# Kernel tuning notes

Measured on AMD Instinct MI355X. Metric: run time of the kernel, lower is better.

The kernel has to match this reference:

```python
import jax, jax.numpy as jnp
import numpy as np


def _layernorm(x, g, b):
    # keras LayerNormalization default epsilon = 1e-3
    m = jnp.mean(x, axis=-1, keepdims=True)
    v = jnp.var(x, axis=-1, keepdims=True)
    return (x - m) * jax.lax.rsqrt(v + 1e-3) * g + b


def _gat(x, mask, W, a_src, a_dst, b):
    # PyG-style GATConv with concat heads, expressed densely over the
    # thresholded adjacency mask (edges where adj > 0.5; mask[i, j] = edge j->i).
    # x: [B, N, Din], W: [Din, H, C], mask: [N, N] bool
    h = jnp.einsum('bnd,dhc->bnhc', x, W)                 # [B,N,H,C]
    s_src = jnp.einsum('bnhc,hc->bhn', h, a_src)          # [B,H,N]
    s_dst = jnp.einsum('bnhc,hc->bhn', h, a_dst)          # [B,H,N]
    e = jax.nn.leaky_relu(s_dst[:, :, :, None] + s_src[:, :, None, :], 0.2)  # [B,H,i,j]
    e = jnp.where(mask[None, None], e, jnp.float32(-1e9))
    alpha = jax.nn.softmax(e, axis=-1)                    # softmax over neighbors j
    out = jnp.einsum('bhij,bjhc->bihc', alpha, h)         # aggregate messages
    B, N, H, C = out.shape
    return out.reshape(B, N, H * C) + b


def setup_inputs() -> dict:
    key = jax.random.key(0)
    ks = jax.random.split(key, 20)
    B, T, N, F = 4, 24, 500, 3
    HID, OUT, HEADS = 8, 16, 4      # SpatialProcessor(num_nodes, 3, 8, 16)
    D, AH, KD, FF = 16, 2, 8, 32    # EfficientTransformer(16, heads=2, ff_dim=32)
    n = lambda k, shape, sc=0.3: jax.random.normal(k, shape, dtype=jnp.float32) * sc
    z = lambda shape: jnp.zeros(shape, jnp.float32)
    return {
        'x': jax.random.normal(ks[0], (B, T, N, F), dtype=jnp.float32),
        'embedding': jax.random.normal(ks[1], (N, HID), dtype=jnp.float32),
        'proj_w': n(ks[2], (F, HID)), 'proj_b': z((HID,)),
        'g1_w': n(ks[3], (HID, HEADS, HID // HEADS)),
        'g1_as': n(ks[4], (HEADS, HID // HEADS)),
        'g1_ad': n(ks[5], (HEADS, HID // HEADS)),
        'g1_b': z((HID,)),
        'g2_w': n(ks[6], (HID, HEADS, OUT // HEADS)),
        'g2_as': n(ks[7], (HEADS, OUT // HEADS)),
        'g2_ad': n(ks[8], (HEADS, OUT // HEADS)),
        'g2_b': z((OUT,)),
        'wq': n(ks[9], (D, AH, KD)), 'bq': z((AH, KD)),
        'wk': n(ks[10], (D, AH, KD)), 'bk': z((AH, KD)),
        'wv': n(ks[11], (D, AH, KD)), 'bv': z((AH, KD)),
        'wo': n(ks[12], (AH, KD, D)), 'bo': z((D,)),
        'ln1_g': jnp.ones((D,), jnp.float32), 'ln1_b': z((D,)),
        'ln2_g': jnp.ones((D,), jnp.float32), 'ln2_b': z((D,)),
        'f_w1': n(ks[13], (D, FF)), 'f_b1': z((FF,)),
        'f_w2': n(ks[14], (FF, D)), 'f_b2': z((D,)),
        'r_w1': n(ks[15], (D, D)), 'r_b1': z((D,)),
        'r_w2': n(ks[16], (D, 1)), 'r_b2': z((1,)),
    }


def reference(x, embedding, proj_w, proj_b, g1_w, g1_as, g1_ad, g1_b,
              g2_w, g2_as, g2_ad, g2_b, wq, bq, wk, bk, wv, bv, wo, bo,
              ln1_g, ln1_b, ln2_g, ln2_b, f_w1, f_b1, f_w2, f_b2,
              r_w1, r_b1, r_w2, r_b2):
    B, T, N, F = x.shape
    # AdaptiveAdjacency: cosine similarity of learned node embeddings,
    # identical across batch; edges extracted where adj > 0.5 (diag is 1 -> self loops)
    ne = embedding * jax.lax.rsqrt(jnp.sum(embedding * embedding, -1, keepdims=True))
    adj = ne @ ne.T
    mask = adj > 0.5                                   # [N, N] bool
    # SpatialProcessor over B*T independent graphs
    h = x.reshape(B * T, N, F) @ proj_w + proj_b        # Dense proj -> [BT, N, 8]
    h = jax.nn.gelu(_gat(h, mask, g1_w, g1_as, g1_ad, g1_b), approximate=False)
    h = _gat(h, mask, g2_w, g2_as, g2_ad, g2_b)         # [BT, N, 16]
    D = h.shape[-1]
    # Faithful to original: raw tf.reshape [B,T,N,16] -> [B*N, T, 16] (no transpose)
    t = h.reshape(B * N, T, D)
    # keras MultiHeadAttention(heads=2, key_dim=8), 1 transformer layer
    q = jnp.einsum('bse,ehd->bshd', t, wq) + bq
    k = jnp.einsum('bse,ehd->bshd', t, wk) + bk
    v = jnp.einsum('bse,ehd->bshd', t, wv) + bv
    scale = jnp.sqrt(jnp.asarray(q.shape[-1], jnp.float32))
    att = jax.nn.softmax(jnp.einsum('bshd,bthd->bhst', q, k) / scale, axis=-1)
    o = jnp.einsum('bhst,bthd->bshd', att, v)
    o = jnp.einsum('bshd,hde->bse', o, wo) + bo
    t = _layernorm(t + o, ln1_g, ln1_b)
    ffn = jax.nn.gelu(t @ f_w1 + f_b1, approximate=False) @ f_w2 + f_b2
    t = _layernorm(t + ffn, ln2_g, ln2_b)
    pooled = t.reshape(B, N, T, D).mean(axis=2)
    r = jax.nn.gelu(pooled @ r_w1 + r_b1, approximate=False) @ r_w2 + r_b2
    return r[..., 0]
```

## Files before the change

### kernel.cpp

```cpp
#include <hip/hip_runtime.h>
#include <math.h>
#include <type_traits>

#define DEV __device__ __forceinline__

DEV float gelu_exact(float x) {
    return 0.5f * x * (1.0f + erff(x * 0.70710678118654752f));
}

__global__ __launch_bounds__(512)
void mask_kernel(const float* __restrict__ emb,
                 unsigned short* __restrict__ nbr,
                 int* __restrict__ deg) {
    const int i = blockIdx.x;
    const int j = threadIdx.x;
    float ei[8], ej[8];
    float si = 0.f, sj = 0.f;
#pragma unroll
    for (int e = 0; e < 8; ++e) { ei[e] = emb[i * 8 + e]; si += ei[e] * ei[e]; }
    const int jj = (j < 500) ? j : 0;
#pragma unroll
    for (int e = 0; e < 8; ++e) { ej[e] = emb[jj * 8 + e]; sj += ej[e] * ej[e]; }
    const float ri = 1.0f / sqrtf(si);
    const float rj = 1.0f / sqrtf(sj);
    float dot = 0.f;
#pragma unroll
    for (int e = 0; e < 8; ++e) dot += (ei[e] * ri) * (ej[e] * rj);
    const bool pred = (j < 500) && (dot > 0.5f);
    const unsigned long long m = __ballot(pred);

    __shared__ unsigned wcnt[8];
    const int wave = j >> 6, lane = j & 63;
    if (lane == 0) wcnt[wave] = (unsigned)__popcll(m);
    __syncthreads();
    unsigned off = 0;
    for (int w = 0; w < wave; ++w) off += wcnt[w];
    if (pred) {
        const unsigned pos = off + (unsigned)__popcll(m & ((1ull << lane) - 1ull));
        if (pos < 128) nbr[i * 128 + pos] = (unsigned short)j;
    }
    if (j == 0) {
        unsigned t = 0;
        for (int w = 0; w < 8; ++w) t += wcnt[w];
        deg[i] = (int)(t > 128u ? 128u : t);
    }
}

template <int C, int OUTS, bool PROJ, bool GELU_OUT>
__global__ __launch_bounds__(512)
void gat_kernel(const float* __restrict__ in,
                const float* __restrict__ pw,
                const float* __restrict__ pb,
                const float* __restrict__ W,
                const float* __restrict__ asrc,
                const float* __restrict__ adst,
                const float* __restrict__ bias,
                const unsigned short* __restrict__ nbr,
                const int* __restrict__ deg,
                float* __restrict__ out) {
    using Vec = std::conditional_t<C == 2, float2, float4>;
    constexpr int HSTR = (C == 2) ? 10 : 20;
    const int b = blockIdx.x >> 3;
    const int slice = blockIdx.x & 7;
    const int tid = threadIdx.x;
    __shared__ float h1[500 * HSTR];
    __shared__ float ssrc[4 * 516];

    if (tid < 500) {
        float xv[8];
        if constexpr (PROJ) {
            const float* xr = in + ((size_t)b * 500 + tid) * 3;
            const float x0 = xr[0], x1 = xr[1], x2 = xr[2];
#pragma unroll
            for (int e = 0; e < 8; ++e)
                xv[e] = x0 * pw[e] + x1 * pw[8 + e] + x2 * pw[16 + e] + pb[e];
        } else {
            const float4* xr = (const float4*)(in + ((size_t)b * 500 + tid) * 8);
            const float4 v0 = xr[0], v1 = xr[1];
            xv[0] = v0.x; xv[1] = v0.y; xv[2] = v0.z; xv[3] = v0.w;
            xv[4] = v1.x; xv[5] = v1.y; xv[6] = v1.z; xv[7] = v1.w;
        }
#pragma unroll
        for (int h = 0; h < 4; ++h) {
            float acc[C];
#pragma unroll
            for (int c = 0; c < C; ++c) acc[c] = 0.f;
#pragma unroll
            for (int e = 0; e < 8; ++e) {
                const float xe = xv[e];
#pragma unroll
                for (int c = 0; c < C; ++c) acc[c] += xe * W[(e * 4 + h) * C + c];
            }
            float ss = 0.f;
            Vec hv;
#pragma unroll
            for (int c = 0; c < C; ++c) ss += acc[c] * asrc[h * C + c];
            if constexpr (C == 2) { hv.x = acc[0]; hv.y = acc[1]; }
            else { hv.x = acc[0]; hv.y = acc[1]; hv.z = acc[2]; hv.w = acc[3]; }
            *(Vec*)&h1[tid * HSTR + h * C] = hv;
            ssrc[h * 516 + tid] = ss;
        }
    }
    __syncthreads();

    const int pairId = tid >> 1;
    const int half = tid & 1;
    const int h = pairId & 3;
    const int local = pairId >> 2;
    const int i = slice * 63 + local;
    const bool valid = (local < 63) && (i < 500);
    float num[C];
#pragma unroll
    for (int c = 0; c < C; ++c) num[c] = 0.f;
    float den = 0.f;
    if (valid) {
        float dd = 0.f;
        {
            const Vec hi = *(const Vec*)&h1[i * HSTR + h * C];
            if constexpr (C == 2) dd = hi.x * adst[h * 2] + hi.y * adst[h * 2 + 1];
            else dd = hi.x * adst[h * 4] + hi.y * adst[h * 4 + 1] +
                      hi.z * adst[h * 4 + 2] + hi.w * adst[h * 4 + 3];
        }
        const int dg = deg[i];
        const int k0 = half ? (dg >> 1) : 0;
        const int k1 = half ? dg : (dg >> 1);
        const unsigned short* nb = nbr + i * 128;
        const float* sr = ssrc + h * 516;
        int k = k0;
        for (; k + 4 <= k1; k += 4) {
            const int j0 = nb[k], j1 = nb[k + 1], j2 = nb[k + 2], j3 = nb[k + 3];
            float e0 = dd + sr[j0]; e0 = (e0 > 0.f) ? e0 : 0.2f * e0;
            float e1 = dd + sr[j1]; e1 = (e1 > 0.f) ? e1 : 0.2f * e1;
            float e2 = dd + sr[j2]; e2 = (e2 > 0.f) ? e2 : 0.2f * e2;
            float e3 = dd + sr[j3]; e3 = (e3 > 0.f) ? e3 : 0.2f * e3;
            const float w0 = __expf(e0), w1 = __expf(e1);
            const float w2 = __expf(e2), w3 = __expf(e3);
            const Vec ha = *(const Vec*)&h1[j0 * HSTR + h * C];
            const Vec hb = *(const Vec*)&h1[j1 * HSTR + h * C];
            const Vec hc = *(const Vec*)&h1[j2 * HSTR + h * C];
            const Vec hd = *(const Vec*)&h1[j3 * HSTR + h * C];
            den += (w0 + w1) + (w2 + w3);
            if constexpr (C == 2) {
                num[0] += (w0 * ha.x + w1 * hb.x) + (w2 * hc.x + w3 * hd.x);
                num[1] += (w0 * ha.y + w1 * hb.y) + (w2 * hc.y + w3 * hd.y);
            } else {
                num[0] += (w0 * ha.x + w1 * hb.x) + (w2 * hc.x + w3 * hd.x);
                num[1] += (w0 * ha.y + w1 * hb.y) + (w2 * hc.y + w3 * hd.y);
                num[2] += (w0 * ha.z + w1 * hb.z) + (w2 * hc.z + w3 * hd.z);
                num[3] += (w0 * ha.w + w1 * hb.w) + (w2 * hc.w + w3 * hd.w);
            }
        }
        for (; k < k1; ++k) {
            const int j = nb[k];
            float e = dd + sr[j];
            e = (e > 0.f) ? e : 0.2f * e;
            const float w = __expf(e);
            den += w;
            const Vec hj = *(const Vec*)&h1[j * HSTR + h * C];
            if constexpr (C == 2) { num[0] += w * hj.x; num[1] += w * hj.y; }
            else { num[0] += w * hj.x; num[1] += w * hj.y;
                   num[2] += w * hj.z; num[3] += w * hj.w; }
        }
    }
    den += __shfl_xor(den, 1);
#pragma unroll
    for (int c = 0; c < C; ++c) num[c] += __shfl_xor(num[c], 1);
    if (valid && half == 0) {
        const float inv = 1.0f / den;
        float* orow = out + ((size_t)b * 500 + i) * OUTS + h * C;
#pragma unroll
        for (int c = 0; c < C; ++c) {
            float v = num[c] * inv + bias[h * C + c];
            if constexpr (GELU_OUT) v = gelu_exact(v);
            orow[c] = v;
        }
    }
}

__global__ __launch_bounds__(64)
void transformer_kernel(const float* __restrict__ tin,
                        const float* __restrict__ wq, const float* __restrict__ bq,
                        const float* __restrict__ wk, const float* __restrict__ bk,
                        const float* __restrict__ wv, const float* __restrict__ bv,
                        const float* __restrict__ wo, const float* __restrict__ bo,
                        const float* __restrict__ ln1g, const float* __restrict__ ln1b,
                        const float* __restrict__ ln2g, const float* __restrict__ ln2b,
                        const float* __restrict__ fw1, const float* __restrict__ fb1,
                        const float* __restrict__ fw2, const float* __restrict__ fb2,
                        const float* __restrict__ rw1, const float* __restrict__ rb1,
                        const float* __restrict__ rw2, const float* __restrict__ rb2,
                        float* __restrict__ outp) {
    const int r = blockIdx.x;
    const int lane = threadIdx.x;
    const int d = lane & 15;
    const int srow = lane >> 4;
    const int f = lane & 31;
    const int s2 = lane >> 5;
    __shared__ float t0[24][16], qs[24][16], ks[24][16], vs[24][16];
    __shared__ float os[24][16], t1[24][16], hid[24][32], pooled[16];

    const float4* row4 = (const float4*)(tin + (size_t)r * 384);
    float4* t04 = (float4*)&t0[0][0];
#pragma unroll 1
    for (int idx = lane; idx < 96; idx += 64) t04[idx] = row4[idx];
    float wqc[16], wkc[16], wvc[16];
#pragma unroll
    for (int e = 0; e < 16; ++e) {
        wqc[e] = wq[e * 16 + d];
        wkc[e] = wk[e * 16 + d];
        wvc[e] = wv[e * 16 + d];
    }
    const float bqv = bq[d], bkv = bk[d], bvv = bv[d];
    __syncthreads();

#pragma unroll 1
    for (int it = 0; it < 6; ++it) {
        const int s = it * 4 + srow;
        const float4 r0 = *(const float4*)&t0[s][0];
        const float4 r1 = *(const float4*)&t0[s][4];
        const float4 r2 = *(const float4*)&t0[s][8];
        const float4 r3 = *(const float4*)&t0[s][12];
        const float te[16] = {r0.x, r0.y, r0.z, r0.w, r1.x, r1.y, r1.z, r1.w,
                              r2.x, r2.y, r2.z, r2.w, r3.x, r3.y, r3.z, r3.w};
        float aq = bqv, ak = bkv, av = bvv;
#pragma unroll
        for (int e = 0; e < 16; ++e) {
            aq += te[e] * wqc[e];
            ak += te[e] * wkc[e];
            av += te[e] * wvc[e];
        }
        qs[s][d] = aq; ks[s][d] = ak; vs[s][d] = av;
    }
    __syncthreads();

    if (lane < 48) {
        const int h = lane / 24, s = lane % 24;
        const float4 q0 = *(const float4*)&qs[s][h * 8];
        const float4 q1 = *(const float4*)&qs[s][h * 8 + 4];
        float sc[24];
        float mx = -1e30f;
#pragma unroll
        for (int t = 0; t < 24; ++t) {
            const float4 k0 = *(const float4*)&ks[t][h * 8];
            const float4 k1 = *(const float4*)&ks[t][h * 8 + 4];
            float a = q0.x * k0.x + q0.y * k0.y + q0.z * k0.z + q0.w * k0.w +
                      q1.x * k1.x + q1.y * k1.y + q1.z * k1.z + q1.w * k1.w;
            a *= 0.35355339059327373f;
            sc[t] = a;
            mx = fmaxf(mx, a);
        }
        float sum = 0.f;
#pragma unroll
        for (int t = 0; t < 24; ++t) { sc[t] = __expf(sc[t] - mx); sum += sc[t]; }
        const float inv = 1.0f / sum;
        float o0x = 0.f, o0y = 0.f, o0z = 0.f, o0w = 0.f;
        float o1x = 0.f, o1y = 0.f, o1z = 0.f, o1w = 0.f;
#pragma unroll
        for (int t = 0; t < 24; ++t) {
            const float4 v0 = *(const float4*)&vs[t][h * 8];
            const float4 v1 = *(const float4*)&vs[t][h * 8 + 4];
            const float w = sc[t];
            o0x += w * v0.x; o0y += w * v0.y; o0z += w * v0.z; o0w += w * v0.w;
            o1x += w * v1.x; o1y += w * v1.y; o1z += w * v1.z; o1w += w * v1.w;
        }
        float4 ov0 = {o0x * inv, o0y * inv, o0z * inv, o0w * inv};
        float4 ov1 = {o1x * inv, o1y * inv, o1z * inv, o1w * inv};
        *(float4*)&os[s][h * 8] = ov0;
        *(float4*)&os[s][h * 8 + 4] = ov1;
    }
    float woc[16];
#pragma unroll
    for (int hd = 0; hd < 16; ++hd) woc[hd] = wo[hd * 16 + d];
    const float bov = bo[d];
    const float g1v = ln1g[d], be1v = ln1b[d];
    __syncthreads();

#pragma unroll 1
    for (int it = 0; it < 6; ++it) {
        const int s = it * 4 + srow;
        const float4 r0 = *(const float4*)&os[s][0];
        const float4 r1 = *(const float4*)&os[s][4];
        const float4 r2 = *(const float4*)&os[s][8];
        const float4 r3 = *(const float4*)&os[s][12];
        const float oe[16] = {r0.x, r0.y, r0.z, r0.w, r1.x, r1.y, r1.z, r1.w,
                              r2.x, r2.y, r2.z, r2.w, r3.x, r3.y, r3.z, r3.w};
        float a = bov;
#pragma unroll
        for (int hd = 0; hd < 16; ++hd) a += oe[hd] * woc[hd];
        const float xv = t0[s][d] + a;
        float s1 = xv, sq = xv * xv;
        s1 += __shfl_xor(s1, 1); sq += __shfl_xor(sq, 1);
        s1 += __shfl_xor(s1, 2); sq += __shfl_xor(sq, 2);
        s1 += __shfl_xor(s1, 4); sq += __shfl_xor(sq, 4);
        s1 += __shfl_xor(s1, 8); sq += __shfl_xor(sq, 8);
        const float mean = s1 * 0.0625f;
        const float var = fmaxf(sq * 0.0625f - mean * mean, 0.f);
        t1[s][d] = (xv - mean) * rsqrtf(var + 1e-3f) * g1v + be1v;
    }
    float f1c[16];
#pragma unroll
    for (int e = 0; e < 16; ++e) f1c[e] = fw1[e * 32 + f];
    const float fb1v = fb1[f];
    __syncthreads();

#pragma unroll 1
    for (int it = 0; it < 12; ++it) {
        const int s = it * 2 + s2;
        const float4 r0 = *(const float4*)&t1[s][0];
        const float4 r1 = *(const float4*)&t1[s][4];
        const float4 r2 = *(const float4*)&t1[s][8];
        const float4 r3 = *(const float4*)&t1[s][12];
        const float te[16] = {r0.x, r0.y, r0.z, r0.w, r1.x, r1.y, r1.z, r1.w,
                              r2.x, r2.y, r2.z, r2.w, r3.x, r3.y, r3.z, r3.w};
        float a = fb1v;
#pragma unroll
        for (int e = 0; e < 16; ++e) a += te[e] * f1c[e];
        hid[s][f] = gelu_exact(a);
    }
    float f2c[32];
#pragma unroll
    for (int ff = 0; ff < 32; ++ff) f2c[ff] = fw2[ff * 16 + d];
    const float fb2v = fb2[d];
    const float g2v = ln2g[d], be2v = ln2b[d];
    __syncthreads();

    float pacc = 0.f;
#pragma unroll 1
    for (int it = 0; it < 6; ++it) {
        const int s = it * 4 + srow;
        float he[32];
#pragma unroll
        for (int q8 = 0; q8 < 8; ++q8) {
            const float4 rv = *(const float4*)&hid[s][q8 * 4];
            he[q8 * 4 + 0] = rv.x; he[q8 * 4 + 1] = rv.y;
            he[q8 * 4 + 2] = rv.z; he[q8 * 4 + 3] = rv.w;
        }
        float a = fb2v;
#pragma unroll
        for (int ff = 0; ff < 32; ++ff) a += he[ff] * f2c[ff];
        const float xv = t1[s][d] + a;
        float s1 = xv, sq = xv * xv;
        s1 += __shfl_xor(s1, 1); sq += __shfl_xor(sq, 1);
        s1 += __shfl_xor(s1, 2); sq += __shfl_xor(sq, 2);
        s1 += __shfl_xor(s1, 4); sq += __shfl_xor(sq, 4);
        s1 += __shfl_xor(s1, 8); sq += __shfl_xor(sq, 8);
        const float mean = s1 * 0.0625f;
        const float var = fmaxf(sq * 0.0625f - mean * mean, 0.f);
        pacc += (xv - mean) * rsqrtf(var + 1e-3f) * g2v + be2v;
    }
    pacc += __shfl_xor(pacc, 16);
    pacc += __shfl_xor(pacc, 32);
    if (lane < 16) pooled[lane] = pacc * (1.0f / 24.0f);
    __syncthreads();

    float partial = 0.f;
    if (lane < 16) {
        float a = rb1[lane];
#pragma unroll
        for (int e = 0; e < 16; ++e) a += pooled[e] * rw1[e * 16 + lane];
        partial = gelu_exact(a) * rw2[lane];
    }
    partial += __shfl_xor(partial, 8);
    partial += __shfl_xor(partial, 4);
    partial += __shfl_xor(partial, 2);
    partial += __shfl_xor(partial, 1);
    if (lane == 0) outp[r] = partial + rb2[0];
}

extern "C" void kernel_launch(void* const* d_in, const int* in_sizes, int n_in,
                              void* d_out, int out_size, void* d_ws, size_t ws_size,
                              hipStream_t stream) {
    const float* x      = (const float*)d_in[0];
    const float* emb    = (const float*)d_in[1];
    const float* proj_w = (const float*)d_in[2];
    const float* proj_b = (const float*)d_in[3];
    const float* g1_w   = (const float*)d_in[4];
    const float* g1_as  = (const float*)d_in[5];
    const float* g1_ad  = (const float*)d_in[6];
    const float* g1_b   = (const float*)d_in[7];
    const float* g2_w   = (const float*)d_in[8];
    const float* g2_as  = (const float*)d_in[9];
    const float* g2_ad  = (const float*)d_in[10];
    const float* g2_b   = (const float*)d_in[11];
    const float* wq = (const float*)d_in[12];
    const float* bq = (const float*)d_in[13];
    const float* wk = (const float*)d_in[14];
    const float* bk = (const float*)d_in[15];
    const float* wv = (const float*)d_in[16];
    const float* bv = (const float*)d_in[17];
    const float* wo = (const float*)d_in[18];
    const float* bo = (const float*)d_in[19];
    const float* ln1g = (const float*)d_in[20];
    const float* ln1b = (const float*)d_in[21];
    const float* ln2g = (const float*)d_in[22];
    const float* ln2b = (const float*)d_in[23];
    const float* fw1 = (const float*)d_in[24];
    const float* fb1 = (const float*)d_in[25];
    const float* fw2 = (const float*)d_in[26];
    const float* fb2 = (const float*)d_in[27];
    const float* rw1 = (const float*)d_in[28];
    const float* rb1 = (const float*)d_in[29];
    const float* rw2 = (const float*)d_in[30];
    const float* rb2 = (const float*)d_in[31];

    unsigned short* nbr = (unsigned short*)d_ws;
    int* deg   = (int*)((char*)d_ws + 131072);
    float* h_g1  = (float*)((char*)d_ws + 135168);
    float* t_buf = (float*)((char*)d_ws + 135168 + 1536000);

    mask_kernel<<<500, 512, 0, stream>>>(emb, nbr, deg);
    gat_kernel<2, 8, true, true><<<768, 512, 0, stream>>>(
        x, proj_w, proj_b, g1_w, g1_as, g1_ad, g1_b, nbr, deg, h_g1);
    gat_kernel<4, 16, false, false><<<768, 512, 0, stream>>>(
        h_g1, nullptr, nullptr, g2_w, g2_as, g2_ad, g2_b, nbr, deg, t_buf);
    transformer_kernel<<<2000, 64, 0, stream>>>(
        t_buf, wq, bq, wk, bk, wv, bv, wo, bo, ln1g, ln1b, ln2g, ln2b,
        fw1, fb1, fw2, fb2, rw1, rb1, rw2, rb2, (float*)d_out);
}
```

Before: 43.70 us.

## Fuse adjacency mask construction into first GAT kernel and swizzle shared h layout

```diff
diff --git a/kernel.cpp b/kernel.cpp
--- a/kernel.cpp
+++ b/kernel.cpp
@@ -8,45 +8,7 @@
     return 0.5f * x * (1.0f + erff(x * 0.70710678118654752f));
 }
 
-__global__ __launch_bounds__(512)
-void mask_kernel(const float* __restrict__ emb,
-                 unsigned short* __restrict__ nbr,
-                 int* __restrict__ deg) {
-    const int i = blockIdx.x;
-    const int j = threadIdx.x;
-    float ei[8], ej[8];
-    float si = 0.f, sj = 0.f;
-#pragma unroll
-    for (int e = 0; e < 8; ++e) { ei[e] = emb[i * 8 + e]; si += ei[e] * ei[e]; }
-    const int jj = (j < 500) ? j : 0;
-#pragma unroll
-    for (int e = 0; e < 8; ++e) { ej[e] = emb[jj * 8 + e]; sj += ej[e] * ej[e]; }
-    const float ri = 1.0f / sqrtf(si);
-    const float rj = 1.0f / sqrtf(sj);
-    float dot = 0.f;
-#pragma unroll
-    for (int e = 0; e < 8; ++e) dot += (ei[e] * ri) * (ej[e] * rj);
-    const bool pred = (j < 500) && (dot > 0.5f);
-    const unsigned long long m = __ballot(pred);
-
-    __shared__ unsigned wcnt[8];
-    const int wave = j >> 6, lane = j & 63;
-    if (lane == 0) wcnt[wave] = (unsigned)__popcll(m);
-    __syncthreads();
-    unsigned off = 0;
-    for (int w = 0; w < wave; ++w) off += wcnt[w];
-    if (pred) {
-        const unsigned pos = off + (unsigned)__popcll(m & ((1ull << lane) - 1ull));
-        if (pos < 128) nbr[i * 128 + pos] = (unsigned short)j;
-    }
-    if (j == 0) {
-        unsigned t = 0;
-        for (int w = 0; w < 8; ++w) t += wcnt[w];
-        deg[i] = (int)(t > 128u ? 128u : t);
-    }
-}
-
-template <int C, int OUTS, bool PROJ, bool GELU_OUT>
+template <int C, int OUTS, bool PROJ, bool GELU_OUT, bool BUILD_CSR>
 __global__ __launch_bounds__(512)
 void gat_kernel(const float* __restrict__ in,
                 const float* __restrict__ pw,
@@ -55,16 +17,88 @@
                 const float* __restrict__ asrc,
                 const float* __restrict__ adst,
                 const float* __restrict__ bias,
-                const unsigned short* __restrict__ nbr,
-                const int* __restrict__ deg,
+                const float* __restrict__ emb,
+                unsigned short* __restrict__ nbr,
+                int* __restrict__ deg,
                 float* __restrict__ out) {
     using Vec = std::conditional_t<C == 2, float2, float4>;
-    constexpr int HSTR = (C == 2) ? 10 : 20;
     const int b = blockIdx.x >> 3;
     const int slice = blockIdx.x & 7;
     const int tid = threadIdx.x;
-    __shared__ float h1[500 * HSTR];
-    __shared__ float ssrc[4 * 516];
+
+    __shared__ float h1f[C == 2 ? 4000 : 8000];
+    __shared__ float ssrc[2000];
+    __shared__ unsigned short nbr_s[BUILD_CSR ? 63 * 128 : 2];
+    __shared__ int deg_s[BUILD_CSR ? 64 : 1];
+
+    if constexpr (BUILD_CSR) {
+        float* ne = h1f;
+        if (tid < 500) {
+            const float4 e0 = *(const float4*)&emb[tid * 8];
+            const float4 e1 = *(const float4*)&emb[tid * 8 + 4];
+            const float n = e0.x * e0.x + e0.y * e0.y + e0.z * e0.z + e0.w * e0.w +
+                            e1.x * e1.x + e1.y * e1.y + e1.z * e1.z + e1.w * e1.w;
+            const float rn = rsqrtf(n);
+            ne[tid * 8 + 0] = e0.x * rn; ne[tid * 8 + 1] = e0.y * rn;
+            ne[tid * 8 + 2] = e0.z * rn; ne[tid * 8 + 3] = e0.w * rn;
+            ne[tid * 8 + 4] = e1.x * rn; ne[tid * 8 + 5] = e1.y * rn;
+            ne[tid * 8 + 6] = e1.z * rn; ne[tid * 8 + 7] = e1.w * rn;
+        }
+        __syncthreads();
+
+        unsigned long long* mask_s = (unsigned long long*)ssrc;
+        const int sub = tid >> 6;
+        const int local = tid & 63;
+        const int i = slice * 63 + local;
+        const bool rvalid = (local < 63) && (i < 500);
+        float nei[8];
+        if (rvalid) {
+#pragma unroll
+            for (int e = 0; e < 8; ++e) nei[e] = ne[i * 8 + e];
+        }
+        unsigned long long bm = 0;
+        const int jbase = sub * 63;
+        const int jend = (jbase + 63 < 500) ? jbase + 63 : 500;
+        for (int j = jbase; j < jend; ++j) {
+            const float4 a = *(const float4*)&ne[j * 8];
+            const float4 c = *(const float4*)&ne[j * 8 + 4];
+            const float dot = nei[0] * a.x + nei[1] * a.y + nei[2] * a.z +
+                              nei[3] * a.w + nei[4] * c.x + nei[5] * c.y +
+                              nei[6] * c.z + nei[7] * c.w;
+            if (rvalid && dot > 0.5f) bm |= 1ull << (j - jbase);
+        }
+        mask_s[local * 8 + sub] = bm;
+        __syncthreads();
+
+        if (rvalid) {
+            int off = 0;
+            for (int s = 0; s < sub; ++s) off += __popcll(mask_s[local * 8 + s]);
+            unsigned long long m = bm;
+            int pos = off;
+            while (m) {
+                const int bit = __ffsll(m) - 1;
+                m &= (m - 1);
+                if (pos < 128) nbr_s[local * 128 + pos] = (unsigned short)(jbase + bit);
+                ++pos;
+            }
+            if (sub == 0) {
+                int t = 0;
+#pragma unroll
+                for (int s = 0; s < 8; ++s) t += __popcll(mask_s[local * 8 + s]);
+                deg_s[local] = (t > 128) ? 128 : t;
+            }
+        }
+        __syncthreads();
+
+        if (b == 0) {
+            for (int t = tid; t < 63 * 128; t += 512) {
+                const int row = t >> 7, k = t & 127;
+                const int gi = slice * 63 + row;
+                if (gi < 500 && k < deg_s[row]) nbr[gi * 128 + k] = nbr_s[row * 128 + k];
+            }
+            if (tid < 63 && slice * 63 + tid < 500) deg[slice * 63 + tid] = deg_s[tid];
+        }
+    }
 
     if (tid < 500) {
         float xv[8];
@@ -92,13 +126,14 @@
                 for (int c = 0; c < C; ++c) acc[c] += xe * W[(e * 4 + h) * C + c];
             }
             float ss = 0.f;
+#pragma unroll
+            for (int c = 0; c < C; ++c) ss += acc[c] * asrc[h * C + c];
             Vec hv;
-#pragma unroll
-            for (int c = 0; c < C; ++c) ss += acc[c] * asrc[h * C + c];
             if constexpr (C == 2) { hv.x = acc[0]; hv.y = acc[1]; }
             else { hv.x = acc[0]; hv.y = acc[1]; hv.z = acc[2]; hv.w = acc[3]; }
-            *(Vec*)&h1[tid * HSTR + h * C] = hv;
-            ssrc[h * 516 + tid] = ss;
+            const int u = tid * 4 + ((h + tid) & 3);
+            *(Vec*)&h1f[u * C] = hv;
+            ssrc[h * 500 + tid] = ss;
         }
     }
     __syncthreads();
@@ -116,16 +151,16 @@
     if (valid) {
         float dd = 0.f;
         {
-            const Vec hi = *(const Vec*)&h1[i * HSTR + h * C];
+            const Vec hi = *(const Vec*)&h1f[(i * 4 + ((h + i) & 3)) * C];
             if constexpr (C == 2) dd = hi.x * adst[h * 2] + hi.y * adst[h * 2 + 1];
             else dd = hi.x * adst[h * 4] + hi.y * adst[h * 4 + 1] +
                       hi.z * adst[h * 4 + 2] + hi.w * adst[h * 4 + 3];
         }
-        const int dg = deg[i];
+        const int dg = BUILD_CSR ? deg_s[local] : deg[i];
+        const unsigned short* nb = BUILD_CSR ? (nbr_s + local * 128) : (nbr + i * 128);
+        const float* sr = ssrc + h * 500;
         const int k0 = half ? (dg >> 1) : 0;
         const int k1 = half ? dg : (dg >> 1);
-        const unsigned short* nb = nbr + i * 128;
-        const float* sr = ssrc + h * 516;
         int k = k0;
         for (; k + 4 <= k1; k += 4) {
             const int j0 = nb[k], j1 = nb[k + 1], j2 = nb[k + 2], j3 = nb[k + 3];
@@ -135,10 +170,10 @@
             float e3 = dd + sr[j3]; e3 = (e3 > 0.f) ? e3 : 0.2f * e3;
             const float w0 = __expf(e0), w1 = __expf(e1);
             const float w2 = __expf(e2), w3 = __expf(e3);
-            const Vec ha = *(const Vec*)&h1[j0 * HSTR + h * C];
-            const Vec hb = *(const Vec*)&h1[j1 * HSTR + h * C];
-            const Vec hc = *(const Vec*)&h1[j2 * HSTR + h * C];
-            const Vec hd = *(const Vec*)&h1[j3 * HSTR + h * C];
+            const Vec ha = *(const Vec*)&h1f[(j0 * 4 + ((h + j0) & 3)) * C];
+            const Vec hb = *(const Vec*)&h1f[(j1 * 4 + ((h + j1) & 3)) * C];
+            const Vec hc = *(const Vec*)&h1f[(j2 * 4 + ((h + j2) & 3)) * C];
+            const Vec hd = *(const Vec*)&h1f[(j3 * 4 + ((h + j3) & 3)) * C];
             den += (w0 + w1) + (w2 + w3);
             if constexpr (C == 2) {
                 num[0] += (w0 * ha.x + w1 * hb.x) + (w2 * hc.x + w3 * hd.x);
@@ -156,7 +191,7 @@
             e = (e > 0.f) ? e : 0.2f * e;
             const float w = __expf(e);
             den += w;
-            const Vec hj = *(const Vec*)&h1[j * HSTR + h * C];
+            const Vec hj = *(const Vec*)&h1f[(j * 4 + ((h + j) & 3)) * C];
             if constexpr (C == 2) { num[0] += w * hj.x; num[1] += w * hj.y; }
             else { num[0] += w * hj.x; num[1] += w * hj.y;
                    num[2] += w * hj.z; num[3] += w * hj.w; }
@@ -408,11 +443,10 @@
     float* h_g1  = (float*)((char*)d_ws + 135168);
     float* t_buf = (float*)((char*)d_ws + 135168 + 1536000);
 
-    mask_kernel<<<500, 512, 0, stream>>>(emb, nbr, deg);
-    gat_kernel<2, 8, true, true><<<768, 512, 0, stream>>>(
-        x, proj_w, proj_b, g1_w, g1_as, g1_ad, g1_b, nbr, deg, h_g1);
-    gat_kernel<4, 16, false, false><<<768, 512, 0, stream>>>(
-        h_g1, nullptr, nullptr, g2_w, g2_as, g2_ad, g2_b, nbr, deg, t_buf);
+    gat_kernel<2, 8, true, true, true><<<768, 512, 0, stream>>>(
+        x, proj_w, proj_b, g1_w, g1_as, g1_ad, g1_b, emb, nbr, deg, h_g1);
+    gat_kernel<4, 16, false, false, false><<<768, 512, 0, stream>>>(
+        h_g1, nullptr, nullptr, g2_w, g2_as, g2_ad, g2_b, nullptr, nbr, deg, t_buf);
     transformer_kernel<<<2000, 64, 0, stream>>>(
         t_buf, wq, bq, wk, bk, wv, bv, wo, bo, ln1g, ln1b, ln2g, ln2b,
         fw1, fb1, fw2, fb2, rw1, rb1, rw2, rb2, (float*)d_out);
```

Result: slower. 57.93 us (+32.6%).
